# Kernel optimization log

Measured on AMD Instinct MI355X. Metric: run time of the kernel, lower is better.

The kernel has to match this reference:

```python
import jax, jax.numpy as jnp
import numpy as np

M, D, G, E = 100000, 64, 1024, 1600000  # nodes, hidden, graphs, edges


def setup_inputs() -> dict:
    key = jax.random.key(0)
    k1, k2, k3, k4 = jax.random.split(key, 4)
    x = jax.random.normal(k1, (M, D), dtype=jnp.float32)
    batch = jnp.sort(jax.random.randint(k2, (M,), 0, G)).astype(jnp.int64)
    edge = jax.random.randint(k3, (2, E), 0, M).astype(jnp.int64)
    # nn.Linear(D, 1) parameters
    att_w = jax.random.normal(k4, (1, D), dtype=jnp.float32) * (1.0 / np.sqrt(D))
    att_b = jnp.zeros((1,), dtype=jnp.float32)
    return {"x": x, "att_w": att_w, "att_b": att_b, "batch": batch, "edge": edge}


def reference(x, att_w, att_b, batch, edge):
    # imp = attention(x): [M, 1] -> [M]
    imp = (x @ att_w.T + att_b)[:, 0]
    # scatter_softmax of imp over graph segments (batch)
    seg_max = jax.ops.segment_max(imp, batch, num_segments=G)
    e = jnp.exp(imp - seg_max[batch])
    denom = jax.ops.segment_sum(e, batch, num_segments=G)
    a = e / denom[batch]  # [M]
    # (degree branch is dead code when degree=False; degree softmax unused)
    # per-node weighted outer product imp_k * x_k x_k^T, scatter-summed per graph
    wj = (a[:, None] * x)[:, :, None] * x[:, None, :]  # [M, D, D]
    out = jax.ops.segment_sum(wj, batch, num_segments=G)  # [G, D, D]
    # Triuvec: upper-triangular (incl. diagonal) vectorization, row-major
    iu = jnp.triu_indices(D)
    return out[:, iu[0], iu[1]]  # [G, D*(D+1)/2]
```

## Files before the change

### kernel.cpp

```cpp
#include <hip/hip_runtime.h>
#include <math.h>


#define DDIM 64
#define NTRI 2080
#define CAP  1024
#define TILE 32

__global__ void __launch_bounds__(256)
prep_kernel(const float* __restrict__ x,
            const float* __restrict__ att_w,
            const float* __restrict__ att_b,
            const int*   __restrict__ batch,
            float*       __restrict__ imp,
            int*         __restrict__ seg_start,
            int M, int G)
{
    const int tid    = threadIdx.x;
    const int lane16 = tid & 15;
    const int node   = blockIdx.x * 16 + (tid >> 4);

    if (node < M) {
        const float4 v = ((const float4*)x)[node * 16 + lane16];
        const float4 w = ((const float4*)att_w)[lane16];
        float d = fmaf(v.x, w.x, fmaf(v.y, w.y, fmaf(v.z, w.z, v.w * w.w)));
        d += __shfl_down(d, 8, 16);
        d += __shfl_down(d, 4, 16);
        d += __shfl_down(d, 2, 16);
        d += __shfl_down(d, 1, 16);
        if (lane16 == 0) imp[node] = d + att_b[0];
    }
    if (tid < 16) {
        const int m = blockIdx.x * 16 + tid;
        if (m < M) {
            const int b0 = batch[m];
            if (m == 0) {
                for (int g = 0; g <= b0; ++g) seg_start[g] = 0;
            } else {
                const int bp = batch[m - 1];
                for (int g = bp + 1; g <= b0; ++g) seg_start[g] = m;
            }
            if (m == M - 1) {
                for (int g = b0 + 1; g <= G; ++g) seg_start[g] = M;
            }
        }
    }
}

__global__ void __launch_bounds__(256)
sop_kernel(const float* __restrict__ x,
           const float* __restrict__ imp,
           const int*   __restrict__ seg_start,
           float*       __restrict__ out,
           int M)
{
    const int g   = blockIdx.x;
    const int tid = threadIdx.x;

    __shared__ float sA[CAP];
    __shared__ float sX[2][TILE * DDIM];
    __shared__ float sAt[2][TILE];
    __shared__ float sRed[8];

    const int s = seg_start[g];
    const int e = seg_start[g + 1];
    const int n = e - s;
    float* og = out + (size_t)g * NTRI;

    if (n == 0) {
        for (int i = tid; i < NTRI; i += 256) og[i] = 0.f;
        return;
    }

    float lmax = -INFINITY;
    for (int i = tid; i < n; i += 256) lmax = fmaxf(lmax, imp[s + i]);
#pragma unroll
    for (int off = 32; off > 0; off >>= 1) lmax = fmaxf(lmax, __shfl_down(lmax, off, 64));
    const int wid = tid >> 6, lane = tid & 63;
    if (lane == 0) sRed[wid] = lmax;
    __syncthreads();
    if (tid == 0) sRed[4] = fmaxf(fmaxf(sRed[0], sRed[1]), fmaxf(sRed[2], sRed[3]));
    __syncthreads();
    const float mx = sRed[4];

    float lsum = 0.f;
    for (int i = tid; i < n; i += 256) {
        const float ev = __expf(imp[s + i] - mx);
        if (i < CAP) sA[i] = ev;
        lsum += ev;
    }
#pragma unroll
    for (int off = 32; off > 0; off >>= 1) lsum += __shfl_down(lsum, off, 64);
    if (lane == 0) sRed[wid] = lsum;
    __syncthreads();
    if (tid == 0) sRed[5] = 1.0f / (sRed[0] + sRed[1] + sRed[2] + sRed[3]);
    __syncthreads();
    const float inv = sRed[5];

    const int ty = tid >> 4, tx = tid & 15;
    const int i0 = ty * 4, j0 = tx * 4;
    float acc[4][4];
#pragma unroll
    for (int a = 0; a < 4; ++a)
#pragma unroll
        for (int b = 0; b < 4; ++b) acc[a][b] = 0.f;

    const float4* x4 = (const float4*)x;
    const int T = (n + TILE - 1) / TILE;

    float4 r0, r1;
    {
        const int nt0 = min(TILE, n);
        const long base = (long)s * 16;
        const float4 z = {0.f, 0.f, 0.f, 0.f};
        r0 = (tid       < nt0 * 16) ? x4[base + tid]       : z;
        r1 = (tid + 256 < nt0 * 16) ? x4[base + tid + 256] : z;
    }

    for (int t = 0; t < T; ++t) {
        const int t0  = t * TILE;
        const int nt  = min(TILE, n - t0);
        const int cur = t & 1;

        ((float4*)sX[cur])[tid]       = r0;
        ((float4*)sX[cur])[tid + 256] = r1;
        if (tid < TILE) {
            const int gidx = t0 + tid;
            float av = 0.f;
            if (gidx < n)
                av = ((gidx < CAP) ? sA[gidx] : __expf(imp[s + gidx] - mx)) * inv;
            sAt[cur][tid] = av;
        }
        if (t + 1 < T) {
            const int t0n = t0 + TILE;
            const int ntn = min(TILE, n - t0n);
            const long base = (long)(s + t0n) * 16;
            const float4 z = {0.f, 0.f, 0.f, 0.f};
            r0 = (tid       < ntn * 16) ? x4[base + tid]       : z;
            r1 = (tid + 256 < ntn * 16) ? x4[base + tid + 256] : z;
        }
        __syncthreads();

        const float* xb = sX[cur];
        const float* ab = sAt[cur];
        if (nt == TILE) {
#pragma unroll 8
            for (int nn = 0; nn < TILE; ++nn) {
                const float c  = ab[nn];
                const float4 xi = *(const float4*)&xb[nn * DDIM + i0];
                const float4 xj = *(const float4*)&xb[nn * DDIM + j0];
                const float yv[4] = {c * xi.x, c * xi.y, c * xi.z, c * xi.w};
                const float xv[4] = {xj.x, xj.y, xj.z, xj.w};
#pragma unroll
                for (int a = 0; a < 4; ++a)
#pragma unroll
                    for (int b = 0; b < 4; ++b)
                        acc[a][b] = fmaf(yv[a], xv[b], acc[a][b]);
            }
        } else {
            for (int nn = 0; nn < nt; ++nn) {
                const float c  = ab[nn];
                const float4 xi = *(const float4*)&xb[nn * DDIM + i0];
                const float4 xj = *(const float4*)&xb[nn * DDIM + j0];
                const float yv[4] = {c * xi.x, c * xi.y, c * xi.z, c * xi.w};
                const float xv[4] = {xj.x, xj.y, xj.z, xj.w};
#pragma unroll
                for (int a = 0; a < 4; ++a)
#pragma unroll
                    for (int b = 0; b < 4; ++b)
                        acc[a][b] = fmaf(yv[a], xv[b], acc[a][b]);
            }
        }
    }

#pragma unroll
    for (int a = 0; a < 4; ++a) {
        const int i = i0 + a;
        const int base = i * DDIM - (i * (i - 1)) / 2;
#pragma unroll
        for (int b = 0; b < 4; ++b) {
            const int j = j0 + b;
            if (j >= i) og[base + (j - i)] = acc[a][b];
        }
    }
}

extern "C" void kernel_launch(void* const* d_in, const int* in_sizes, int n_in,
                              void* d_out, int out_size, void* d_ws, size_t ws_size,
                              hipStream_t stream) {
    const float* x     = (const float*)d_in[0];
    const float* att_w = (const float*)d_in[1];
    const float* att_b = (const float*)d_in[2];
    const int*   batch = (const int*)d_in[3];
    float* out = (float*)d_out;

    const int M = in_sizes[0] / DDIM;
    const int G = out_size / NTRI;

    int*   seg_start = (int*)d_ws;
    float* imp       = (float*)((char*)d_ws + 8192);

    const int blocksA = (M + 15) / 16;
    prep_kernel<<<blocksA, 256, 0, stream>>>(x, att_w, att_b, batch, imp, seg_start, M, G);
    sop_kernel<<<G, 256, 0, stream>>>(x, imp, seg_start, out, M);
}
```

Before: 102.7 us.

## Fuse attention score into per-graph kernel and split node loop across wavefronts

The attention dot product moves from the prep kernel into the per-graph kernel, which computes scores from x while reading each segment, so the global imp buffer round trip goes away. Each wavefront now handles a quarter of the nodes with an 8x8 register tile covering the full 64x64 product, and the four partial results are summed through shared memory at the end. The attention weight is folded into a precomputed scaled copy of x in shared memory. In exchange x for each segment is read an extra time, register pressure rises to 64 accumulators, and there is a cross-wave reduction step.

```diff
diff --git a/kernel.cpp b/kernel.cpp
--- a/kernel.cpp
+++ b/kernel.cpp
@@ -7,64 +7,54 @@
 #define CAP  1024
 #define TILE 32
 
+__device__ __forceinline__ float dot_row_w(const float* __restrict__ row,
+                                           const float* __restrict__ sW) {
+    float d = 0.f;
+#pragma unroll
+    for (int k = 0; k < 16; ++k) {
+        const float4 v = ((const float4*)row)[k];
+        const float4 w = ((const float4*)sW)[k];
+        d = fmaf(v.x, w.x, d); d = fmaf(v.y, w.y, d);
+        d = fmaf(v.z, w.z, d); d = fmaf(v.w, w.w, d);
+    }
+    return d;
+}
+
 __global__ void __launch_bounds__(256)
-prep_kernel(const float* __restrict__ x,
-            const float* __restrict__ att_w,
-            const float* __restrict__ att_b,
-            const int*   __restrict__ batch,
-            float*       __restrict__ imp,
-            int*         __restrict__ seg_start,
-            int M, int G)
+bounds_kernel(const int* __restrict__ batch, int* __restrict__ seg_start, int M, int G)
 {
-    const int tid    = threadIdx.x;
-    const int lane16 = tid & 15;
-    const int node   = blockIdx.x * 16 + (tid >> 4);
-
-    if (node < M) {
-        const float4 v = ((const float4*)x)[node * 16 + lane16];
-        const float4 w = ((const float4*)att_w)[lane16];
-        float d = fmaf(v.x, w.x, fmaf(v.y, w.y, fmaf(v.z, w.z, v.w * w.w)));
-        d += __shfl_down(d, 8, 16);
-        d += __shfl_down(d, 4, 16);
-        d += __shfl_down(d, 2, 16);
-        d += __shfl_down(d, 1, 16);
-        if (lane16 == 0) imp[node] = d + att_b[0];
-    }
-    if (tid < 16) {
-        const int m = blockIdx.x * 16 + tid;
-        if (m < M) {
-            const int b0 = batch[m];
-            if (m == 0) {
-                for (int g = 0; g <= b0; ++g) seg_start[g] = 0;
-            } else {
-                const int bp = batch[m - 1];
-                for (int g = bp + 1; g <= b0; ++g) seg_start[g] = m;
-            }
-            if (m == M - 1) {
-                for (int g = b0 + 1; g <= G; ++g) seg_start[g] = M;
-            }
-        }
-    }
-}
-
-__global__ void __launch_bounds__(256)
+    const int m = blockIdx.x * 256 + threadIdx.x;
+    if (m >= M) return;
+    const int b0 = batch[m];
+    if (m == 0) {
+        for (int g = 0; g <= b0; ++g) seg_start[g] = 0;
+    } else {
+        const int bp = batch[m - 1];
+        for (int g = bp + 1; g <= b0; ++g) seg_start[g] = m;
+    }
+    if (m == M - 1) {
+        for (int g = b0 + 1; g <= G; ++g) seg_start[g] = M;
+    }
+}
+
+__global__ void __launch_bounds__(256, 4)
 sop_kernel(const float* __restrict__ x,
-           const float* __restrict__ imp,
+           const float* __restrict__ att_w,
+           const float* __restrict__ att_b,
            const int*   __restrict__ seg_start,
-           float*       __restrict__ out,
-           int M)
+           float*       __restrict__ out)
 {
+    __shared__ __align__(16) float smem[CAP + 4 * TILE * DDIM + DDIM];
+    float* sA  = smem;
+    float* sXr = smem + CAP;
+    float* sYs = smem + CAP + 2 * TILE * DDIM;
+    float* sW  = smem + CAP + 4 * TILE * DDIM;
+    __shared__ float sRed[8];
+
     const int g   = blockIdx.x;
     const int tid = threadIdx.x;
-
-    __shared__ float sA[CAP];
-    __shared__ float sX[2][TILE * DDIM];
-    __shared__ float sAt[2][TILE];
-    __shared__ float sRed[8];
-
-    const int s = seg_start[g];
-    const int e = seg_start[g + 1];
-    const int n = e - s;
+    const int s   = seg_start[g];
+    const int n   = seg_start[g + 1] - s;
     float* og = out + (size_t)g * NTRI;
 
     if (n == 0) {
@@ -72,11 +62,32 @@
         return;
     }
 
+    const int lane16 = tid & 15;
+    const int grp    = tid >> 4;
+    const float4 wv  = ((const float4*)att_w)[lane16];
+    const float  bb  = att_b[0];
+    if (tid < DDIM) sW[tid] = att_w[tid];
+    const float4* x4 = (const float4*)x;
+
+    for (int idx = grp; idx < n; idx += 16) {
+        const float4 v = x4[(size_t)(s + idx) * 16 + lane16];
+        float d = fmaf(v.x, wv.x, fmaf(v.y, wv.y, fmaf(v.z, wv.z, v.w * wv.w)));
+        d += __shfl_xor(d, 1, 16);
+        d += __shfl_xor(d, 2, 16);
+        d += __shfl_xor(d, 4, 16);
+        d += __shfl_xor(d, 8, 16);
+        if (lane16 == 0 && idx < CAP) sA[idx] = d + bb;
+    }
+    __syncthreads();
+
+    const int wid = tid >> 6, lane = tid & 63;
     float lmax = -INFINITY;
-    for (int i = tid; i < n; i += 256) lmax = fmaxf(lmax, imp[s + i]);
+    for (int i = tid; i < n; i += 256) {
+        const float d = (i < CAP) ? sA[i] : (dot_row_w(x + (size_t)(s + i) * DDIM, sW) + bb);
+        lmax = fmaxf(lmax, d);
+    }
 #pragma unroll
     for (int off = 32; off > 0; off >>= 1) lmax = fmaxf(lmax, __shfl_down(lmax, off, 64));
-    const int wid = tid >> 6, lane = tid & 63;
     if (lane == 0) sRed[wid] = lmax;
     __syncthreads();
     if (tid == 0) sRed[4] = fmaxf(fmaxf(sRed[0], sRed[1]), fmaxf(sRed[2], sRed[3]));
@@ -85,7 +96,8 @@
 
     float lsum = 0.f;
     for (int i = tid; i < n; i += 256) {
-        const float ev = __expf(imp[s + i] - mx);
+        const float d  = (i < CAP) ? sA[i] : (dot_row_w(x + (size_t)(s + i) * DDIM, sW) + bb);
+        const float ev = __expf(d - mx);
         if (i < CAP) sA[i] = ev;
         lsum += ev;
     }
@@ -96,22 +108,22 @@
     if (tid == 0) sRed[5] = 1.0f / (sRed[0] + sRed[1] + sRed[2] + sRed[3]);
     __syncthreads();
     const float inv = sRed[5];
-
-    const int ty = tid >> 4, tx = tid & 15;
-    const int i0 = ty * 4, j0 = tx * 4;
-    float acc[4][4];
-#pragma unroll
-    for (int a = 0; a < 4; ++a)
-#pragma unroll
-        for (int b = 0; b < 4; ++b) acc[a][b] = 0.f;
-
-    const float4* x4 = (const float4*)x;
+    for (int i = tid; i < n && i < CAP; i += 256) sA[i] *= inv;
+    __syncthreads();
+
+    const int i0 = (lane & 7) * 8;
+    const int j0 = (lane >> 3) * 8;
+    float acc[8][8];
+#pragma unroll
+    for (int a = 0; a < 8; ++a)
+#pragma unroll
+        for (int b = 0; b < 8; ++b) acc[a][b] = 0.f;
+
     const int T = (n + TILE - 1) / TILE;
-
     float4 r0, r1;
     {
         const int nt0 = min(TILE, n);
-        const long base = (long)s * 16;
+        const size_t base = (size_t)s * 16;
         const float4 z = {0.f, 0.f, 0.f, 0.f};
         r0 = (tid       < nt0 * 16) ? x4[base + tid]       : z;
         r1 = (tid + 256 < nt0 * 16) ? x4[base + tid + 256] : z;
@@ -121,66 +133,96 @@
         const int t0  = t * TILE;
         const int nt  = min(TILE, n - t0);
         const int cur = t & 1;
-
-        ((float4*)sX[cur])[tid]       = r0;
-        ((float4*)sX[cur])[tid + 256] = r1;
-        if (tid < TILE) {
-            const int gidx = t0 + tid;
-            float av = 0.f;
-            if (gidx < n)
-                av = ((gidx < CAP) ? sA[gidx] : __expf(imp[s + gidx] - mx)) * inv;
-            sAt[cur][tid] = av;
+        float* xb = sXr + cur * TILE * DDIM;
+        float* yb = sYs + cur * TILE * DDIM;
+
+        {
+            const int g0 = t0 + (tid >> 4);
+            const int g1 = t0 + ((tid + 256) >> 4);
+            float c0 = 0.f, c1 = 0.f;
+            if (g0 < n) c0 = (g0 < CAP) ? sA[g0] : __expf(dot_row_w(x + (size_t)(s + g0) * DDIM, sW) + bb - mx) * inv;
+            if (g1 < n) c1 = (g1 < CAP) ? sA[g1] : __expf(dot_row_w(x + (size_t)(s + g1) * DDIM, sW) + bb - mx) * inv;
+            ((float4*)xb)[tid]       = r0;
+            ((float4*)xb)[tid + 256] = r1;
+            float4 y0 = {c0 * r0.x, c0 * r0.y, c0 * r0.z, c0 * r0.w};
+            float4 y1 = {c1 * r1.x, c1 * r1.y, c1 * r1.z, c1 * r1.w};
+            ((float4*)yb)[tid]       = y0;
+            ((float4*)yb)[tid + 256] = y1;
         }
         if (t + 1 < T) {
             const int t0n = t0 + TILE;
             const int ntn = min(TILE, n - t0n);
-            const long base = (long)(s + t0n) * 16;
+            const size_t base = (size_t)(s + t0n) * 16;
             const float4 z = {0.f, 0.f, 0.f, 0.f};
             r0 = (tid       < ntn * 16) ? x4[base + tid]       : z;
             r1 = (tid + 256 < ntn * 16) ? x4[base + tid + 256] : z;
         }
         __syncthreads();
 
-        const float* xb = sX[cur];
-        const float* ab = sAt[cur];
-        if (nt == TILE) {
-#pragma unroll 8
-            for (int nn = 0; nn < TILE; ++nn) {
-                const float c  = ab[nn];
-                const float4 xi = *(const float4*)&xb[nn * DDIM + i0];
-                const float4 xj = *(const float4*)&xb[nn * DDIM + j0];
-                const float yv[4] = {c * xi.x, c * xi.y, c * xi.z, c * xi.w};
-                const float xv[4] = {xj.x, xj.y, xj.z, xj.w};
-#pragma unroll
-                for (int a = 0; a < 4; ++a)
-#pragma unroll
-                    for (int b = 0; b < 4; ++b)
-                        acc[a][b] = fmaf(yv[a], xv[b], acc[a][b]);
-            }
-        } else {
-            for (int nn = 0; nn < nt; ++nn) {
-                const float c  = ab[nn];
-                const float4 xi = *(const float4*)&xb[nn * DDIM + i0];
-                const float4 xj = *(const float4*)&xb[nn * DDIM + j0];
-                const float yv[4] = {c * xi.x, c * xi.y, c * xi.z, c * xi.w};
-                const float xv[4] = {xj.x, xj.y, xj.z, xj.w};
-#pragma unroll
-                for (int a = 0; a < 4; ++a)
-#pragma unroll
-                    for (int b = 0; b < 4; ++b)
-                        acc[a][b] = fmaf(yv[a], xv[b], acc[a][b]);
-            }
-        }
-    }
-
+        for (int nn = wid; nn < nt; nn += 4) {
+            float yv[8], xv[8];
+            *(float4*)&yv[0] = *(const float4*)&yb[nn * DDIM + i0];
+            *(float4*)&yv[4] = *(const float4*)&yb[nn * DDIM + i0 + 4];
+            *(float4*)&xv[0] = *(const float4*)&xb[nn * DDIM + j0];
+            *(float4*)&xv[4] = *(const float4*)&xb[nn * DDIM + j0 + 4];
+#pragma unroll
+            for (int a = 0; a < 8; ++a)
+#pragma unroll
+                for (int b = 0; b < 8; ++b)
+                    acc[a][b] = fmaf(yv[a], xv[b], acc[a][b]);
+        }
+    }
+    __syncthreads();
+
+    float* red0 = smem;
+    float* red1 = smem + 4096;
+    if (wid == 0) {
+#pragma unroll
+        for (int a = 0; a < 8; ++a) {
+            *(float4*)&red0[(i0 + a) * DDIM + j0]     = *(const float4*)&acc[a][0];
+            *(float4*)&red0[(i0 + a) * DDIM + j0 + 4] = *(const float4*)&acc[a][4];
+        }
+    } else if (wid == 1) {
+#pragma unroll
+        for (int a = 0; a < 8; ++a) {
+            *(float4*)&red1[(i0 + a) * DDIM + j0]     = *(const float4*)&acc[a][0];
+            *(float4*)&red1[(i0 + a) * DDIM + j0 + 4] = *(const float4*)&acc[a][4];
+        }
+    }
+    __syncthreads();
+    if (wid == 2) {
+#pragma unroll
+        for (int a = 0; a < 8; ++a) {
+            float4 u = *(const float4*)&red0[(i0 + a) * DDIM + j0];
+            float4 v = *(const float4*)&red0[(i0 + a) * DDIM + j0 + 4];
+            u.x += acc[a][0]; u.y += acc[a][1]; u.z += acc[a][2]; u.w += acc[a][3];
+            v.x += acc[a][4]; v.y += acc[a][5]; v.z += acc[a][6]; v.w += acc[a][7];
+            *(float4*)&red0[(i0 + a) * DDIM + j0]     = u;
+            *(float4*)&red0[(i0 + a) * DDIM + j0 + 4] = v;
+        }
+    } else if (wid == 3) {
+#pragma unroll
+        for (int a = 0; a < 8; ++a) {
+            float4 u = *(const float4*)&red1[(i0 + a) * DDIM + j0];
+            float4 v = *(const float4*)&red1[(i0 + a) * DDIM + j0 + 4];
+            u.x += acc[a][0]; u.y += acc[a][1]; u.z += acc[a][2]; u.w += acc[a][3];
+            v.x += acc[a][4]; v.y += acc[a][5]; v.z += acc[a][6]; v.w += acc[a][7];
+            *(float4*)&red1[(i0 + a) * DDIM + j0]     = u;
+            *(float4*)&red1[(i0 + a) * DDIM + j0 + 4] = v;
+        }
+    }
+    __syncthreads();
+
+    const int ty = tid >> 4, tx = tid & 15;
+    const int fi0 = ty * 4, fj0 = tx * 4;
 #pragma unroll
     for (int a = 0; a < 4; ++a) {
-        const int i = i0 + a;
+        const int i = fi0 + a;
         const int base = i * DDIM - (i * (i - 1)) / 2;
 #pragma unroll
         for (int b = 0; b < 4; ++b) {
-            const int j = j0 + b;
-            if (j >= i) og[base + (j - i)] = acc[a][b];
+            const int j = fj0 + b;
+            if (j >= i) og[base + (j - i)] = red0[i * DDIM + j] + red1[i * DDIM + j];
         }
     }
 }
@@ -197,10 +239,8 @@
     const int M = in_sizes[0] / DDIM;
     const int G = out_size / NTRI;
 
-    int*   seg_start = (int*)d_ws;
-    float* imp       = (float*)((char*)d_ws + 8192);
-
-    const int blocksA = (M + 15) / 16;
-    prep_kernel<<<blocksA, 256, 0, stream>>>(x, att_w, att_b, batch, imp, seg_start, M, G);
-    sop_kernel<<<G, 256, 0, stream>>>(x, imp, seg_start, out, M);
-}
+    int* seg_start = (int*)d_ws;
+
+    bounds_kernel<<<(M + 255) / 256, 256, 0, stream>>>(batch, seg_start, M, G);
+    sop_kernel<<<G, 256, 0, stream>>>(x, att_w, att_b, seg_start, out);
+}
```

Result: slower. 108.5 us (+5.7%).
